# Kernel optimization log

Measured on AMD Instinct MI355X. Metric: run time of the kernel, lower is better.

## Reference

```python
import jax, jax.numpy as jnp
import numpy as np

B, S, D_IN, D_H, D_ACT = 16, 2048, 1024, 2048, 1024


def setup_inputs() -> dict:
    key = jax.random.key(0)
    ks = jax.random.split(key, 8)
    s_in = 1.0 / np.sqrt(D_IN)
    s_h = 1.0 / np.sqrt(D_H)
    return {
        "x": jax.random.normal(ks[0], (B, S, D_IN), dtype=jnp.float32),
        "W_init": jax.random.uniform(ks[1], (D_H, D_IN), jnp.float32, -s_in, s_in),
        "b_init": jax.random.uniform(ks[2], (D_H,), jnp.float32, -s_in, s_in),
        "W_ih": jax.random.uniform(ks[3], (D_H, D_H), jnp.float32, -s_h, s_h),
        "b_ih": jax.random.uniform(ks[4], (D_H,), jnp.float32, -s_h, s_h),
        "b_hh": jax.random.uniform(ks[5], (D_H,), jnp.float32, -s_h, s_h),
        "W_final": jax.random.uniform(ks[6], (D_ACT, D_H), jnp.float32, -s_h, s_h),
        "b_final": jax.random.uniform(ks[7], (D_ACT,), jnp.float32, -s_h, s_h),
    }


def reference(x, W_init, b_init, W_ih, b_ih, b_hh, W_final, b_final):
    # initial linear + relu: [B,S,D_IN] -> [B,S,D_H]
    h = jax.nn.relu(jnp.einsum('bsi,hi->bsh', x, W_init) + b_init)
    # per-timestep RNN with hidden reset to zero each step: the W_hh term
    # vanishes, so each step is relu(W_ih @ h_t + b_ih + b_hh) -> one GEMM.
    out = jax.nn.relu(jnp.einsum('bsh,gh->bsg', h, W_ih) + b_ih + b_hh)
    # final linear: [B,S,D_H] -> [B,S,D_ACT]
    return jnp.einsum('bsh,ah->bsa', out, W_final) + b_final
```

## Files before the change

kernel.cpp:

```cpp
#include <hip/hip_runtime.h>
#include <hip/hip_bf16.h>
#include <stdint.h>
#include <stddef.h>

typedef __bf16 bf16;
typedef __bf16 bf16x8 __attribute__((ext_vector_type(8)));
typedef float f32x4 __attribute__((ext_vector_type(4)));
typedef __attribute__((address_space(1))) void gvoid;
typedef __attribute__((address_space(3))) void lvoid;

#define FENCE() asm volatile("" ::: "memory")
#define VMCNT(n) asm volatile("s_waitcnt vmcnt(" #n ")" ::: "memory")
#define BARS() do { FENCE(); __builtin_amdgcn_s_barrier(); FENCE(); } while (0)

__global__ __launch_bounds__(256)
void cvt_f32_bf16(const float* __restrict__ in, bf16* __restrict__ out, int n8)
{
    int i = blockIdx.x * 256 + threadIdx.x;
    if (i >= n8) return;
    const f32x4* p = (const f32x4*)in + (size_t)i * 2;
    f32x4 a = p[0], b = p[1];
    bf16x8 o;
    o[0] = (bf16)a[0]; o[1] = (bf16)a[1]; o[2] = (bf16)a[2]; o[3] = (bf16)a[3];
    o[4] = (bf16)b[0]; o[5] = (bf16)b[1]; o[6] = (bf16)b[2]; o[7] = (bf16)b[3];
    *((bf16x8*)out + i) = o;
}

#define RDA(buf, mh) \
    _Pragma("unroll") \
    for (int m_ = 0; m_ < 4; ++m_) { \
        const int r_ = ((mh) + m_) * 16 + frow; \
        af[m_][0] = *(const bf16x8*)&As[(buf)*16384 + wr*8192 + r_*64 + ((fg     ^ (r_ & 7)) * 8)]; \
        af[m_][1] = *(const bf16x8*)&As[(buf)*16384 + wr*8192 + r_*64 + (((fg+4) ^ (r_ & 7)) * 8)]; \
    }

#define RDB(buf, dst, nb) \
    _Pragma("unroll") \
    for (int n_ = 0; n_ < 2; ++n_) { \
        const int r_ = (wc & 1) * 64 + ((nb) + n_) * 16 + frow; \
        dst[n_][0] = *(const bf16x8*)&Bs[(buf)*16384 + (wc>>1)*8192 + r_*64 + ((fg     ^ (r_ & 7)) * 8)]; \
        dst[n_][1] = *(const bf16x8*)&Bs[(buf)*16384 + (wc>>1)*8192 + r_*64 + (((fg+4) ^ (r_ & 7)) * 8)]; \
    }

#define STAGE(gsrc, lreg, h, kt) do { \
        const bf16* g_ = (gsrc) + (size_t)((h) * 128) * K + (size_t)(kt) * 64; \
        bf16* l_ = (lreg) + (h) * 8192 + wave * 1024; \
        __builtin_amdgcn_global_load_lds((gvoid*)g_,           (lvoid*)l_,         16, 0, 0); \
        __builtin_amdgcn_global_load_lds((gvoid*)(g_ + rowK8), (lvoid*)(l_ + 512), 16, 0, 0); \
    } while (0)

#define QUAD(mh, nh, bb) \
    _Pragma("unroll") \
    for (int m_ = 0; m_ < 4; ++m_) \
        _Pragma("unroll") \
        for (int n_ = 0; n_ < 2; ++n_) { \
            acc[(mh)+m_][(nh)+n_] = __builtin_amdgcn_mfma_f32_16x16x32_bf16( \
                af[m_][0], bb[n_][0], acc[(mh)+m_][(nh)+n_], 0, 0, 0); \
            acc[(mh)+m_][(nh)+n_] = __builtin_amdgcn_mfma_f32_16x16x32_bf16( \
                af[m_][1], bb[n_][1], acc[(mh)+m_][(nh)+n_], 0, 0, 0); \
        }

template<int RELU, int TWO_BIAS, int OUTF32>
__global__ __launch_bounds__(512, 2)
void gemm256(const bf16* __restrict__ A, const bf16* __restrict__ Bm,
             const float* __restrict__ bias1, const float* __restrict__ bias2,
             void* __restrict__ Cp, int M, int N, int K)
{
    extern __shared__ bf16 smem[];
    bf16* As = smem;
    bf16* Bs = smem + 32768;

    const int tid  = threadIdx.x;
    const int wave = tid >> 6;
    const int lane = tid & 63;
    const int wr   = wave >> 2;
    const int wc   = wave & 3;
    const int bn = blockIdx.x;
    const int bm = blockIdx.y;

    const int rc  = lane >> 3;
    const int sgc = ((lane & 7) ^ rc) * 8;
    const bf16* aS0 = A  + (size_t)(bm * 256 + wave * 16 + rc) * K + sgc;
    const bf16* bS0 = Bm + (size_t)(bn * 256 + wave * 16 + rc) * K + sgc;
    const size_t rowK8 = (size_t)8 * K;

    const int frow = lane & 15;
    const int fg   = lane >> 4;

    bf16x8 af[4][2], bl[2][2], bh[2][2];
    f32x4 acc[8][4];
    #pragma unroll
    for (int i = 0; i < 8; ++i)
        #pragma unroll
        for (int j = 0; j < 4; ++j)
            acc[i][j] = {0.f, 0.f, 0.f, 0.f};

    const int NT = K >> 6;
    const int NI = NT >> 1;

    STAGE(bS0, Bs,         0, 0); STAGE(bS0, Bs,         1, 0);
    STAGE(aS0, As,         0, 0); STAGE(aS0, As,         1, 0);
    STAGE(bS0, Bs + 16384, 0, 1); STAGE(bS0, Bs + 16384, 1, 1);
    VMCNT(4);
    BARS();

    for (int it = 0; it < NI; ++it) {
        const int t1 = 2 * it + 1;
        const int t2 = (2 * it + 2 < NT) ? 2 * it + 2 : 0;
        const int t3 = t2 + 1;

        RDA(0, 0);
        RDB(0, bl, 0);
        STAGE(aS0, As + 16384, 0, t1);
        BARS();
        __builtin_amdgcn_s_setprio(1); QUAD(0, 0, bl); __builtin_amdgcn_s_setprio(0);
        BARS();
        RDB(0, bh, 2);
        STAGE(aS0, As + 16384, 1, t1);
        BARS();
        __builtin_amdgcn_s_setprio(1); QUAD(0, 2, bh); __builtin_amdgcn_s_setprio(0);
        BARS();
        RDA(0, 4);
        STAGE(bS0, Bs, 0, t2);
        BARS();
        __builtin_amdgcn_s_setprio(1); QUAD(4, 0, bl); __builtin_amdgcn_s_setprio(0);
        BARS();
        STAGE(bS0, Bs, 1, t2);
        VMCNT(4);
        BARS();
        __builtin_amdgcn_s_setprio(1); QUAD(4, 2, bh); __builtin_amdgcn_s_setprio(0);
        BARS();
        RDA(1, 0);
        RDB(1, bl, 0);
        STAGE(aS0, As, 0, t2);
        BARS();
        __builtin_amdgcn_s_setprio(1); QUAD(0, 0, bl); __builtin_amdgcn_s_setprio(0);
        BARS();
        RDB(1, bh, 2);
        STAGE(aS0, As, 1, t2);
        BARS();
        __builtin_amdgcn_s_setprio(1); QUAD(0, 2, bh); __builtin_amdgcn_s_setprio(0);
        BARS();
        RDA(1, 4);
        STAGE(bS0, Bs + 16384, 0, t3);
        BARS();
        __builtin_amdgcn_s_setprio(1); QUAD(4, 0, bl); __builtin_amdgcn_s_setprio(0);
        BARS();
        STAGE(bS0, Bs + 16384, 1, t3);
        VMCNT(4);
        BARS();
        __builtin_amdgcn_s_setprio(1); QUAD(4, 2, bh); __builtin_amdgcn_s_setprio(0);
        BARS();
    }
    VMCNT(0);

    const int crow0 = bm * 256 + wr * 128 + (lane >> 4) * 4;
    const int ccol0 = bn * 256 + wc * 64 + (lane & 15);

    #pragma unroll
    for (int n = 0; n < 4; ++n) {
        const int col = ccol0 + n * 16;
        float bv = bias1[col];
        if (TWO_BIAS) bv += bias2[col];
        #pragma unroll
        for (int m = 0; m < 8; ++m) {
            const int row = crow0 + m * 16;
            #pragma unroll
            for (int r = 0; r < 4; ++r) {
                float v = acc[m][n][r] + bv;
                if (RELU) v = fmaxf(v, 0.0f);
                if (OUTF32)
                    ((float*)Cp)[(size_t)(row + r) * N + col] = v;
                else
                    ((bf16*)Cp)[(size_t)(row + r) * N + col] = (bf16)v;
            }
        }
    }
}

static inline int cvt_blocks(size_t n) { return (int)((n / 8 + 255) / 256); }

extern "C" void kernel_launch(void* const* d_in, const int* in_sizes, int n_in,
                              void* d_out, int out_size, void* d_ws, size_t ws_size,
                              hipStream_t stream) {
    const float* x       = (const float*)d_in[0];
    const float* W_init  = (const float*)d_in[1];
    const float* b_init  = (const float*)d_in[2];
    const float* W_ih    = (const float*)d_in[3];
    const float* b_ih    = (const float*)d_in[4];
    const float* b_hh    = (const float*)d_in[5];
    const float* W_final = (const float*)d_in[6];
    const float* b_final = (const float*)d_in[7];
    float* out = (float*)d_out;

    const int D_H   = in_sizes[2];
    const int D_IN  = in_sizes[1] / D_H;
    const int D_ACT = in_sizes[7];
    const int M     = in_sizes[0] / D_IN;

    const size_t nx  = (size_t)M * D_IN;
    const size_t nw1 = (size_t)D_H * D_IN;
    const size_t nw2 = (size_t)D_H * D_H;
    const size_t nw3 = (size_t)D_ACT * D_H;
    const size_t nh  = (size_t)M * D_H;

    char* ws  = (char*)d_ws;
    bf16* h   = (bf16*)ws;
    bf16* a2  = (bf16*)(ws + nh * 2);
    bf16* xb  = a2;
    bf16* w1b = (bf16*)(ws + nh * 4);
    bf16* w2b = w1b + nw1;
    bf16* w3b = w2b + nw2;

    (void)hipFuncSetAttribute(reinterpret_cast<const void*>(&gemm256<1, 0, 0>),
                              hipFuncAttributeMaxDynamicSharedMemorySize, 131072);
    (void)hipFuncSetAttribute(reinterpret_cast<const void*>(&gemm256<1, 1, 0>),
                              hipFuncAttributeMaxDynamicSharedMemorySize, 131072);
    (void)hipFuncSetAttribute(reinterpret_cast<const void*>(&gemm256<0, 0, 1>),
                              hipFuncAttributeMaxDynamicSharedMemorySize, 131072);

    cvt_f32_bf16<<<cvt_blocks(nx),  256, 0, stream>>>(x,       xb,  (int)(nx  / 8));
    cvt_f32_bf16<<<cvt_blocks(nw1), 256, 0, stream>>>(W_init,  w1b, (int)(nw1 / 8));
    cvt_f32_bf16<<<cvt_blocks(nw2), 256, 0, stream>>>(W_ih,    w2b, (int)(nw2 / 8));
    cvt_f32_bf16<<<cvt_blocks(nw3), 256, 0, stream>>>(W_final, w3b, (int)(nw3 / 8));

    gemm256<1, 0, 0><<<dim3(D_H / 256, M / 256), 512, 131072, stream>>>(
        xb, w1b, b_init, nullptr, h, M, D_H, D_IN);

    gemm256<1, 1, 0><<<dim3(D_H / 256, M / 256), 512, 131072, stream>>>(
        h, w2b, b_ih, b_hh, a2, M, D_H, D_H);

    gemm256<0, 0, 1><<<dim3(D_ACT / 256, M / 256), 512, 131072, stream>>>(
        a2, w3b, b_final, nullptr, out, M, D_ACT, D_H);
}
```

Baseline: 777.9 us.

## Trim GEMM barriers, remap workgroups for L2 locality, reorder MFMA and epilogue

Drops the barrier after each MFMA phase and moves some global-to-LDS stages after compute, so the main loop runs with about half as many workgroup barriers. Adds an XCD-aware remap of workgroup IDs so that neighbouring tiles land on the same L2 slice. It also reorders the MFMAs by K-half, which changes accumulator dependency distance, and restructures the epilogue loop. Removing barriers carries a risk of LDS read/write races between the ds_reads and the async stages into the same buffers.

```diff
diff --git a/kernel.cpp b/kernel.cpp
--- a/kernel.cpp
+++ b/kernel.cpp
@@ -28,19 +28,23 @@
 
 #define RDA(buf, mh) \
     _Pragma("unroll") \
-    for (int m_ = 0; m_ < 4; ++m_) { \
-        const int r_ = ((mh) + m_) * 16 + frow; \
-        af[m_][0] = *(const bf16x8*)&As[(buf)*16384 + wr*8192 + r_*64 + ((fg     ^ (r_ & 7)) * 8)]; \
-        af[m_][1] = *(const bf16x8*)&As[(buf)*16384 + wr*8192 + r_*64 + (((fg+4) ^ (r_ & 7)) * 8)]; \
-    }
+    for (int h_ = 0; h_ < 2; ++h_) \
+        _Pragma("unroll") \
+        for (int m_ = 0; m_ < 4; ++m_) { \
+            const int r_ = ((mh) + m_) * 16 + frow; \
+            af[m_][h_] = *(const bf16x8*)&As[(buf)*16384 + wr*8192 + r_*64 \
+                                            + (((fg + 4*h_) ^ (r_ & 7)) * 8)]; \
+        }
 
 #define RDB(buf, dst, nb) \
     _Pragma("unroll") \
-    for (int n_ = 0; n_ < 2; ++n_) { \
-        const int r_ = (wc & 1) * 64 + ((nb) + n_) * 16 + frow; \
-        dst[n_][0] = *(const bf16x8*)&Bs[(buf)*16384 + (wc>>1)*8192 + r_*64 + ((fg     ^ (r_ & 7)) * 8)]; \
-        dst[n_][1] = *(const bf16x8*)&Bs[(buf)*16384 + (wc>>1)*8192 + r_*64 + (((fg+4) ^ (r_ & 7)) * 8)]; \
-    }
+    for (int h_ = 0; h_ < 2; ++h_) \
+        _Pragma("unroll") \
+        for (int n_ = 0; n_ < 2; ++n_) { \
+            const int r_ = (wc & 1) * 64 + ((nb) + n_) * 16 + frow; \
+            dst[n_][h_] = *(const bf16x8*)&Bs[(buf)*16384 + (wc>>1)*8192 + r_*64 \
+                                             + (((fg + 4*h_) ^ (r_ & 7)) * 8)]; \
+        }
 
 #define STAGE(gsrc, lreg, h, kt) do { \
         const bf16* g_ = (gsrc) + (size_t)((h) * 128) * K + (size_t)(kt) * 64; \
@@ -51,14 +55,17 @@
 
 #define QUAD(mh, nh, bb) \
     _Pragma("unroll") \
-    for (int m_ = 0; m_ < 4; ++m_) \
+    for (int h_ = 0; h_ < 2; ++h_) \
         _Pragma("unroll") \
-        for (int n_ = 0; n_ < 2; ++n_) { \
-            acc[(mh)+m_][(nh)+n_] = __builtin_amdgcn_mfma_f32_16x16x32_bf16( \
-                af[m_][0], bb[n_][0], acc[(mh)+m_][(nh)+n_], 0, 0, 0); \
-            acc[(mh)+m_][(nh)+n_] = __builtin_amdgcn_mfma_f32_16x16x32_bf16( \
-                af[m_][1], bb[n_][1], acc[(mh)+m_][(nh)+n_], 0, 0, 0); \
-        }
+        for (int m_ = 0; m_ < 4; ++m_) \
+            _Pragma("unroll") \
+            for (int n_ = 0; n_ < 2; ++n_) \
+                acc[(mh)+m_][(nh)+n_] = __builtin_amdgcn_mfma_f32_16x16x32_bf16( \
+                    af[m_][h_], bb[n_][h_], acc[(mh)+m_][(nh)+n_], 0, 0, 0);
+
+#define MFMA_PH(mh, nh, bb) do { \
+        __builtin_amdgcn_s_setprio(1); QUAD(mh, nh, bb); __builtin_amdgcn_s_setprio(0); \
+    } while (0)
 
 template<int RELU, int TWO_BIAS, int OUTF32>
 __global__ __launch_bounds__(512, 2)
@@ -75,8 +82,12 @@
     const int lane = tid & 63;
     const int wr   = wave >> 2;
     const int wc   = wave & 3;
-    const int bn = blockIdx.x;
-    const int bm = blockIdx.y;
+
+    const int nwg = gridDim.x * gridDim.y;
+    int wg = blockIdx.y * gridDim.x + blockIdx.x;
+    wg = (wg & 7) * (nwg >> 3) + (wg >> 3);
+    const int bn = wg % gridDim.x;
+    const int bm = wg / gridDim.x;
 
     const int rc  = lane >> 3;
     const int sgc = ((lane & 7) ^ rc) * 8;
@@ -109,70 +120,66 @@
         const int t2 = (2 * it + 2 < NT) ? 2 * it + 2 : 0;
         const int t3 = t2 + 1;
 
+        RDB(0, bl, 0);
         RDA(0, 0);
-        RDB(0, bl, 0);
         STAGE(aS0, As + 16384, 0, t1);
         BARS();
-        __builtin_amdgcn_s_setprio(1); QUAD(0, 0, bl); __builtin_amdgcn_s_setprio(0);
-        BARS();
+        MFMA_PH(0, 0, bl);
         RDB(0, bh, 2);
         STAGE(aS0, As + 16384, 1, t1);
         BARS();
-        __builtin_amdgcn_s_setprio(1); QUAD(0, 2, bh); __builtin_amdgcn_s_setprio(0);
-        BARS();
+        MFMA_PH(0, 2, bh);
         RDA(0, 4);
+        BARS();
+        MFMA_PH(4, 0, bl);
         STAGE(bS0, Bs, 0, t2);
-        BARS();
-        __builtin_amdgcn_s_setprio(1); QUAD(4, 0, bl); __builtin_amdgcn_s_setprio(0);
-        BARS();
         STAGE(bS0, Bs, 1, t2);
         VMCNT(4);
         BARS();
-        __builtin_amdgcn_s_setprio(1); QUAD(4, 2, bh); __builtin_amdgcn_s_setprio(0);
-        BARS();
+        MFMA_PH(4, 2, bh);
+        RDB(1, bl, 0);
         RDA(1, 0);
-        RDB(1, bl, 0);
         STAGE(aS0, As, 0, t2);
         BARS();
-        __builtin_amdgcn_s_setprio(1); QUAD(0, 0, bl); __builtin_amdgcn_s_setprio(0);
-        BARS();
+        MFMA_PH(0, 0, bl);
         RDB(1, bh, 2);
         STAGE(aS0, As, 1, t2);
         BARS();
-        __builtin_amdgcn_s_setprio(1); QUAD(0, 2, bh); __builtin_amdgcn_s_setprio(0);
-        BARS();
+        MFMA_PH(0, 2, bh);
         RDA(1, 4);
+        BARS();
+        MFMA_PH(4, 0, bl);
         STAGE(bS0, Bs + 16384, 0, t3);
-        BARS();
-        __builtin_amdgcn_s_setprio(1); QUAD(4, 0, bl); __builtin_amdgcn_s_setprio(0);
-        BARS();
         STAGE(bS0, Bs + 16384, 1, t3);
         VMCNT(4);
         BARS();
-        __builtin_amdgcn_s_setprio(1); QUAD(4, 2, bh); __builtin_amdgcn_s_setprio(0);
-        BARS();
+        MFMA_PH(4, 2, bh);
     }
     VMCNT(0);
 
     const int crow0 = bm * 256 + wr * 128 + (lane >> 4) * 4;
     const int ccol0 = bn * 256 + wc * 64 + (lane & 15);
 
+    float bv[4];
     #pragma unroll
     for (int n = 0; n < 4; ++n) {
-        const int col = ccol0 + n * 16;
-        float bv = bias1[col];
-        if (TWO_BIAS) bv += bias2[col];
+        bv[n] = bias1[ccol0 + n * 16];
+        if (TWO_BIAS) bv[n] += bias2[ccol0 + n * 16];
+    }
+
+    #pragma unroll
+    for (int m = 0; m < 8; ++m) {
         #pragma unroll
-        for (int m = 0; m < 8; ++m) {
-            const int row = crow0 + m * 16;
+        for (int r = 0; r < 4; ++r) {
+            const size_t row = (size_t)(crow0 + m * 16 + r);
             #pragma unroll
-            for (int r = 0; r < 4; ++r) {
-                float v = acc[m][n][r] + bv;
+            for (int n = 0; n < 4; ++n) {
+                float v = acc[m][n][r] + bv[n];
                 if (RELU) v = fmaxf(v, 0.0f);
                 if (OUTF32)
-                    ((float*)Cp)[(size_t)(row + r) * N + col] = v;
+                    ((float*)Cp)[row * N + ccol0 + n * 16] = v;
                 else
-                    ((bf16*)Cp)[(size_t)(row + r) * N + col] = (bf16)v;
+                    ((bf16*)Cp)[row * N + ccol0 + n * 16] = (bf16)v;
             }
         }
     }
```

Result: faster. 702.6 us (-9.7%).
